# Performance work log

Hardware: AMD Instinct MI355X
Metric: run time of the kernel (lower is better)

## Reference

```python
import jax, jax.numpy as jnp
import numpy as np

NUM_HARMONICS = 64
SAMPLE_RATE = 48000
TWO_PI = 2.0 * np.pi


def setup_inputs() -> dict:
    key = jax.random.key(0)
    k1, k2, k3 = jax.random.split(key, 3)
    B, N, H = 8, 96000, NUM_HARMONICS
    # f0 in a realistic vocal/instrument range ~ [80, 480] Hz
    f0_hz = 80.0 + 400.0 * jax.random.uniform(k1, (B, N), dtype=jnp.float32)
    amp_harm = jax.random.uniform(k2, (B, N, H), dtype=jnp.float32)
    phase = jax.random.normal(k3, (B, H), dtype=jnp.float32)
    return {"f0_hz": f0_hz, "amp_harm": amp_harm, "phase": phase}


def reference(f0_hz, amp_harm, phase):
    # f0_hz: (B, N); amp_harm: (B, N, H); phase: (B, H)
    H = amp_harm.shape[-1]
    omega = (TWO_PI / SAMPLE_RATE) * f0_hz                      # (B, N)
    harm_idx = jnp.arange(1, H + 1, dtype=f0_hz.dtype)          # (H,)
    omega_h = omega[..., None] * harm_idx                       # (B, N, H)
    phases = jnp.cumsum(omega_h, axis=1) + phase[:, None, :]    # (B, N, H)
    y = jnp.einsum('bnh,bnh->bn', amp_harm, jnp.sin(phases))    # (B, N)
    phase_out = jnp.remainder(phases[:, -1, :], TWO_PI)         # (B, H)
    return (y, phase_out)
```

## Files before the change

### kernel.cpp

```cpp
#include <hip/hip_runtime.h>
#include <cstdint>
#include <cstddef>


#define B   8
#define N   96000
#define H   64
#define CH  768
#define NCH 125
#define G   3
#define PF  8

static_assert(CH * NCH == N, "chunking");
static_assert(G * 256 == CH, "scan layout");
static_assert(NCH <= 128, "predecessor spin uses 2 loads/lane");

static constexpr double TWO_PI_D     = 6.2831853071795864769252867665590057684;
static constexpr double INV_TWO_PI_D = 1.0 / TWO_PI_D;
static constexpr double OMEGA_D      = TWO_PI_D / 48000.0;

__device__ __forceinline__ float wrap2pi_f(double v) {
  double r = v - TWO_PI_D * floor(v * INV_TWO_PI_D);
  return (float)r;
}

__global__ __launch_bounds__(256, 4) void k_fused(const float* __restrict__ f0,
                                                  const float* __restrict__ amp,
                                                  const float* __restrict__ phase,
                                                  double* __restrict__ csum,
                                                  float* __restrict__ out) {
  const int blk = blockIdx.x;
  const int b = blk / NCH, c = blk - b * NCH;
  const int tid = threadIdx.x;
  const int lane = tid & 63, wv = tid >> 6;
  const size_t base = (size_t)b * N + (size_t)c * CH;

  __shared__ float  s_w[CH];
  __shared__ double s_warp[4];
  __shared__ double s_pre;
  __shared__ double s_last;

  const float* f0p = f0 + base;
  const float f0v0 = f0p[tid * G + 0];
  const float f0v1 = f0p[tid * G + 1];
  const float f0v2 = f0p[tid * G + 2];

  const int hq = lane & 15;
  const int sl = lane >> 4;
  const float4* ampb = reinterpret_cast<const float4*>(amp) + base * (H / 4);
  float4 pf[PF];
#pragma unroll
  for (int j = 0; j < PF; ++j) {
    const int nl = j * 16 + (wv << 2) + sl;
    pf[j] = ampb[(size_t)nl * (H / 4) + hq];
  }

  const double l0 = OMEGA_D * (double)f0v0;
  const double l1 = OMEGA_D * (double)f0v1;
  const double l2 = OMEGA_D * (double)f0v2;
  const double ts = l0 + l1 + l2;

  double x = ts;
#pragma unroll
  for (int off = 1; off < 64; off <<= 1) {
    double y = __shfl_up(x, off);
    if (lane >= off) x += y;
  }
  if (lane == 63) s_warp[wv] = x;
  __syncthreads();
  if (tid == 0) {
    double a = 0.0;
#pragma unroll
    for (int w = 0; w < 4; ++w) { double t = s_warp[w]; s_warp[w] = a; a += t; }
    __hip_atomic_store(&csum[blk], a, __ATOMIC_RELAXED, __HIP_MEMORY_SCOPE_AGENT);
  }
  __syncthreads();

  if (wv == 0) {
    const double* cs = csum + b * NCH;
    const bool need0 = (lane < c);
    const bool need1 = (lane + 64 < c);
    double v0 = 0.0, v1 = 0.0;
    for (;;) {
      if (need0 && v0 == 0.0)
        v0 = __hip_atomic_load(&cs[lane], __ATOMIC_RELAXED,
                               __HIP_MEMORY_SCOPE_AGENT);
      if (need1 && v1 == 0.0)
        v1 = __hip_atomic_load(&cs[lane + 64], __ATOMIC_RELAXED,
                               __HIP_MEMORY_SCOPE_AGENT);
      const int done = ((!need0) | (v0 != 0.0)) & ((!need1) | (v1 != 0.0));
      if (__all(done)) break;
      __builtin_amdgcn_s_sleep(2);
    }
    double pre = v0 + v1;
    for (int off = 32; off > 0; off >>= 1) pre += __shfl_xor(pre, off);
    if (lane == 0) s_pre = pre;
  }
  __syncthreads();

  const double run = s_pre + s_warp[wv] + (x - ts);
  const double o0 = run + l0;
  const double o1 = o0 + l1;
  const double o2 = o1 + l2;
  s_w[tid * G + 0] = wrap2pi_f(o0);
  s_w[tid * G + 1] = wrap2pi_f(o1);
  s_w[tid * G + 2] = wrap2pi_f(o2);
  if (tid == 255) s_last = o2;
  __syncthreads();

  const float m0 = (float)(hq * 4 + 1), m1 = (float)(hq * 4 + 2);
  const float m2 = (float)(hq * 4 + 3), m3 = (float)(hq * 4 + 4);
  const float* phb = phase + b * H;
  const float p0 = phb[hq * 4 + 0], p1 = phb[hq * 4 + 1];
  const float p2 = phb[hq * 4 + 2], p3 = phb[hq * 4 + 3];
  float* yb = out + base;

#pragma unroll
  for (int j = 0; j < PF; ++j) {
    const int nl = j * 16 + (wv << 2) + sl;
    const float w = s_w[nl];
    const float4 a4 = pf[j];
    float acc;
    acc  = a4.x * __sinf(fmaf(w, m0, p0));
    acc += a4.y * __sinf(fmaf(w, m1, p1));
    acc += a4.z * __sinf(fmaf(w, m2, p2));
    acc += a4.w * __sinf(fmaf(w, m3, p3));
    acc += __shfl_xor(acc, 1);
    acc += __shfl_xor(acc, 2);
    acc += __shfl_xor(acc, 4);
    acc += __shfl_xor(acc, 8);
    if (hq == 0) yb[nl] = acc;
  }

#pragma unroll 4
  for (int i0 = PF * 16; i0 < CH; i0 += 16) {
    const int nl = i0 + (wv << 2) + sl;
    const float w = s_w[nl];
    const float4 a4 = ampb[(size_t)nl * (H / 4) + hq];
    float acc;
    acc  = a4.x * __sinf(fmaf(w, m0, p0));
    acc += a4.y * __sinf(fmaf(w, m1, p1));
    acc += a4.z * __sinf(fmaf(w, m2, p2));
    acc += a4.w * __sinf(fmaf(w, m3, p3));
    acc += __shfl_xor(acc, 1);
    acc += __shfl_xor(acc, 2);
    acc += __shfl_xor(acc, 4);
    acc += __shfl_xor(acc, 8);
    if (hq == 0) yb[nl] = acc;
  }

  if (c == NCH - 1 && tid < H) {
    const double arg = s_last * (double)(tid + 1) + (double)phase[b * H + tid];
    double r = arg - TWO_PI_D * floor(arg * INV_TWO_PI_D);
    if (r < 0.0) r += TWO_PI_D;
    if (r >= TWO_PI_D) r -= TWO_PI_D;
    out[(size_t)B * N + b * H + tid] = (float)r;
  }
}

extern "C" void kernel_launch(void* const* d_in, const int* in_sizes, int n_in,
                              void* d_out, int out_size, void* d_ws, size_t ws_size,
                              hipStream_t stream) {
  const float* f0    = (const float*)d_in[0];
  const float* amp   = (const float*)d_in[1];
  const float* phase = (const float*)d_in[2];
  float* out = (float*)d_out;
  double* csum = (double*)d_ws;

  hipMemsetAsync(d_ws, 0, (size_t)B * NCH * sizeof(double), stream);
  k_fused<<<B * NCH, 256, 0, stream>>>(f0, amp, phase, csum, out);
}
```

Measured before the change: 45.02 us.

## Use 384-thread blocks and publish chunk sum before intra-wave scan

Changes the block from 256 to 384 threads (6 waves), with each thread owning 2 samples loaded as a float2. The chunk total is now computed by a wave-level xor reduction and published to the lookback array before the intra-wave prefix scan runs, so successor blocks can stop spinning sooner. This also removes one __syncthreads. Prefetch depth per wave drops to 4 and the occupancy hint rises to 6 blocks, which may raise register pressure or change how well memory latency is hidden.

```diff
diff --git a/kernel.cpp b/kernel.cpp
--- a/kernel.cpp
+++ b/kernel.cpp
@@ -8,11 +8,13 @@
 #define H   64
 #define CH  768
 #define NCH 125
-#define G   3
-#define PF  8
+#define TM  384
+#define NWV 6
+#define GM  2
+#define PF  4
 
 static_assert(CH * NCH == N, "chunking");
-static_assert(G * 256 == CH, "scan layout");
+static_assert(TM * GM == CH, "scan layout");
 static_assert(NCH <= 128, "predecessor spin uses 2 loads/lane");
 
 static constexpr double TWO_PI_D     = 6.2831853071795864769252867665590057684;
@@ -24,11 +26,11 @@
   return (float)r;
 }
 
-__global__ __launch_bounds__(256, 4) void k_fused(const float* __restrict__ f0,
-                                                  const float* __restrict__ amp,
-                                                  const float* __restrict__ phase,
-                                                  double* __restrict__ csum,
-                                                  float* __restrict__ out) {
+__global__ __launch_bounds__(TM, 6) void k_fused(const float* __restrict__ f0,
+                                                 const float* __restrict__ amp,
+                                                 const float* __restrict__ phase,
+                                                 double* __restrict__ csum,
+                                                 float* __restrict__ out) {
   const int blk = blockIdx.x;
   const int b = blk / NCH, c = blk - b * NCH;
   const int tid = threadIdx.x;
@@ -36,14 +38,11 @@
   const size_t base = (size_t)b * N + (size_t)c * CH;
 
   __shared__ float  s_w[CH];
-  __shared__ double s_warp[4];
+  __shared__ double s_wsum[NWV];
   __shared__ double s_pre;
   __shared__ double s_last;
 
-  const float* f0p = f0 + base;
-  const float f0v0 = f0p[tid * G + 0];
-  const float f0v1 = f0p[tid * G + 1];
-  const float f0v2 = f0p[tid * G + 2];
+  const float2 f0v = reinterpret_cast<const float2*>(f0 + base)[tid];
 
   const int hq = lane & 15;
   const int sl = lane >> 4;
@@ -51,14 +50,25 @@
   float4 pf[PF];
 #pragma unroll
   for (int j = 0; j < PF; ++j) {
-    const int nl = j * 16 + (wv << 2) + sl;
+    const int nl = j * (NWV * 4) + (wv << 2) + sl;
     pf[j] = ampb[(size_t)nl * (H / 4) + hq];
   }
 
-  const double l0 = OMEGA_D * (double)f0v0;
-  const double l1 = OMEGA_D * (double)f0v1;
-  const double l2 = OMEGA_D * (double)f0v2;
-  const double ts = l0 + l1 + l2;
+  const double l0 = OMEGA_D * (double)f0v.x;
+  const double l1 = OMEGA_D * (double)f0v.y;
+  const double ts = l0 + l1;
+
+  double s = ts;
+  for (int off = 32; off > 0; off >>= 1) s += __shfl_xor(s, off);
+  if (lane == 0) s_wsum[wv] = s;
+  __syncthreads();
+  if (tid == 0) {
+    double total = 0.0;
+#pragma unroll
+    for (int w = 0; w < NWV; ++w) total += s_wsum[w];
+    __hip_atomic_store(&csum[blk], total, __ATOMIC_RELAXED,
+                       __HIP_MEMORY_SCOPE_AGENT);
+  }
 
   double x = ts;
 #pragma unroll
@@ -66,15 +76,9 @@
     double y = __shfl_up(x, off);
     if (lane >= off) x += y;
   }
-  if (lane == 63) s_warp[wv] = x;
-  __syncthreads();
-  if (tid == 0) {
-    double a = 0.0;
+  double wavepre = 0.0;
 #pragma unroll
-    for (int w = 0; w < 4; ++w) { double t = s_warp[w]; s_warp[w] = a; a += t; }
-    __hip_atomic_store(&csum[blk], a, __ATOMIC_RELAXED, __HIP_MEMORY_SCOPE_AGENT);
-  }
-  __syncthreads();
+  for (int w = 0; w < NWV - 1; ++w) if (w < wv) wavepre += s_wsum[w];
 
   if (wv == 0) {
     const double* cs = csum + b * NCH;
@@ -98,14 +102,12 @@
   }
   __syncthreads();
 
-  const double run = s_pre + s_warp[wv] + (x - ts);
+  const double run = s_pre + wavepre + (x - ts);
   const double o0 = run + l0;
   const double o1 = o0 + l1;
-  const double o2 = o1 + l2;
-  s_w[tid * G + 0] = wrap2pi_f(o0);
-  s_w[tid * G + 1] = wrap2pi_f(o1);
-  s_w[tid * G + 2] = wrap2pi_f(o2);
-  if (tid == 255) s_last = o2;
+  s_w[tid * GM + 0] = wrap2pi_f(o0);
+  s_w[tid * GM + 1] = wrap2pi_f(o1);
+  if (tid == TM - 1) s_last = o1;
   __syncthreads();
 
   const float m0 = (float)(hq * 4 + 1), m1 = (float)(hq * 4 + 2);
@@ -117,7 +119,7 @@
 
 #pragma unroll
   for (int j = 0; j < PF; ++j) {
-    const int nl = j * 16 + (wv << 2) + sl;
+    const int nl = j * (NWV * 4) + (wv << 2) + sl;
     const float w = s_w[nl];
     const float4 a4 = pf[j];
     float acc;
@@ -133,7 +135,7 @@
   }
 
 #pragma unroll 4
-  for (int i0 = PF * 16; i0 < CH; i0 += 16) {
+  for (int i0 = PF * (NWV * 4); i0 < CH; i0 += NWV * 4) {
     const int nl = i0 + (wv << 2) + sl;
     const float w = s_w[nl];
     const float4 a4 = ampb[(size_t)nl * (H / 4) + hq];
@@ -168,5 +170,5 @@
   double* csum = (double*)d_ws;
 
   hipMemsetAsync(d_ws, 0, (size_t)B * NCH * sizeof(double), stream);
-  k_fused<<<B * NCH, 256, 0, stream>>>(f0, amp, phase, csum, out);
+  k_fused<<<B * NCH, TM, 0, stream>>>(f0, amp, phase, csum, out);
 }
```

New measurement: 43.36 us. -3.7%, faster.
